# Performance work log

Hardware: AMD Instinct MI355X
Metric: run time of the kernel (lower is better)

Reference implementation:

```python
import jax, jax.numpy as jnp
import numpy as np

W = 32            # window_size
HEADS = 8
DH = 64           # dim_head
DIM = 512
NREL = 2 * W - 1  # 63
N = W * W + 1     # 1025 (cls token)
B = 32
EPS = 1e-6
SCALE = DH ** -0.5


def _bias_indices():
    r = np.arange(W)
    gx, gy = np.meshgrid(r, r, indexing='ij')
    grid = np.stack((gx.reshape(-1), gy.reshape(-1)))        # (2, w*w)
    rel = grid[:, :, None] - grid[:, None, :] + (W - 1)       # (2, n, n)
    return (rel[0] * 1 + rel[1] * NREL).astype(np.int32)      # (w*w, w*w)


def setup_inputs() -> dict:
    key = jax.random.key(0)
    ks = jax.random.split(key, 5)
    return {
        'x': jax.random.normal(ks[0], (B, N, DIM), dtype=jnp.float32),
        'w_qkv': jax.random.normal(ks[1], (DIM, 3 * HEADS * DH), dtype=jnp.float32) * 0.02,
        'g': jnp.ones((DH,), dtype=jnp.float32),                      # RMSNorm scale
        'pe_table': jax.random.normal(ks[2], (NREL * NREL, HEADS), dtype=jnp.float32) * 0.02,
        'w_out': jax.random.normal(ks[3], (HEADS * DH, DIM), dtype=jnp.float32) * 0.02,
        'b_out': jnp.zeros((DIM,), dtype=jnp.float32),
        'bias_idx': jnp.asarray(_bias_indices()),
    }


def _rmsnorm(t, g):
    return t * jax.lax.rsqrt(jnp.mean(t * t, axis=-1, keepdims=True) + EPS) * g


def reference(x, w_qkv, g, pe_table, w_out, b_out, bias_idx):
    b, n, _ = x.shape
    # qkv projection; chunk(3) on last dim == leading axis of (3, H, DH)
    qkv = (x @ w_qkv).reshape(b, n, 3, HEADS, DH)
    qkv = jnp.transpose(qkv, (2, 0, 3, 1, 4))                 # (3, b, h, n, d)
    q, k, v = qkv[0], qkv[1], qkv[2]
    dots = jnp.einsum('bhid,bhjd->bhij', _rmsnorm(q, g), _rmsnorm(k, g)) * SCALE
    bias = jnp.transpose(pe_table[bias_idx], (2, 0, 1))       # (h, w*w, w*w)
    dots = dots.at[:, :, 1:, 1:].add(bias)                    # skip cls row/col
    attn = jax.nn.softmax(dots, axis=-1)
    out = jnp.einsum('bhij,bhjd->bhid', attn, v)
    out = jnp.transpose(out, (0, 2, 1, 3)).reshape(b, n, HEADS * DH)
    return out @ w_out + b_out
```

## Files before the change

kernel.cpp:

```cpp
#include <hip/hip_runtime.h>

typedef short bf16x8 __attribute__((ext_vector_type(8)));
typedef float f32x4 __attribute__((ext_vector_type(4)));
typedef float f32x16 __attribute__((ext_vector_type(16)));
typedef unsigned int u32;
typedef u32 u32x4 __attribute__((ext_vector_type(4)));
typedef unsigned short u16;

#define B_    32
#define N_    1025
#define H_    8
#define DIM_  512
#define M_    (B_*N_)
#define QP_   1152
#define BIP_  1152
#define NT_   34
#define KVSZ_ (NT_*2048)
#define BT_   (BIP_*32)
#define SCALE_ 0.125f
#define LOG2E_ 1.4426950408889634f

__device__ __forceinline__ u16 f2bf(float f){
  unsigned u = __builtin_bit_cast(unsigned, f);
  u += 0x7FFFu + ((u >> 16) & 1u);
  return (u16)(u >> 16);
}
__device__ __forceinline__ u32 cvtpk(float a, float b){
  u32 r;
  asm("v_cvt_pk_bf16_f32 %0, %1, %2" : "=v"(r) : "v"(a), "v"(b));
  return r;
}
__device__ __forceinline__ void pswap(u32 &a, u32 &b){
  asm("v_permlane32_swap_b32 %0, %1" : "+v"(a), "+v"(b));
}
__device__ __forceinline__ void gll16(const u16* g, u16* l){
  __builtin_amdgcn_global_load_lds((const __attribute__((address_space(1))) u16*)(g),
                                   (__attribute__((address_space(3))) u16*)(l), 16, 0, 0);
}

__global__ __launch_bounds__(256)
void k_conv_x(const float* __restrict__ x, u16* __restrict__ o, int n4){
  int i = blockIdx.x*256 + threadIdx.x;
  if (i >= n4) return;
  float4 v = ((const float4*)x)[i];
  ushort4 r;
  r.x = f2bf(v.x); r.y = f2bf(v.y); r.z = f2bf(v.z); r.w = f2bf(v.w);
  ((ushort4*)o)[i] = r;
}

__global__ __launch_bounds__(256)
void k_transpose(const float* __restrict__ w, u16* __restrict__ wt, int R, int C){
  int i = blockIdx.x*256 + threadIdx.x;
  if (i >= R*C) return;
  int n = i / R, k = i - n*R;
  wt[i] = f2bf(w[k*C + n]);
}

__global__ __launch_bounds__(256)
void k_biasr(const int* __restrict__ idx, const float* __restrict__ pe, u16* __restrict__ br){
  int i_lin = blockIdx.x*256 + threadIdx.x;
  int v = i_lin & 15, hi = (i_lin>>4)&1;
  int t1 = i_lin >> 5;
  int i = t1 % 1152;
  int t2 = t1 / 1152;
  int tj = t2 % NT_;
  int h = t2 / NT_;
  int j = tj*32 + (v&3) + 8*(v>>2) + 4*hi;
  float val;
  if (j >= 1 && j <= 1024 && i >= 1 && i <= 1024)
    val = pe[idx[(i-1)*1024 + (j-1)]*8 + h] * LOG2E_;
  else
    val = (j <= 1024) ? 0.f : -1e9f;
  br[i_lin] = f2bf(val);
}

__global__ __launch_bounds__(256)
void k_ztail(u16* __restrict__ qn, u16* __restrict__ kn2, u16* __restrict__ v2){
  int i = blockIdx.x*256 + threadIdx.x;
  if (i < 2080768){
    int bh = i / (127*64); int r = i - bh*(127*64);
    qn[((size_t)bh*QP_ + 1025 + (r>>6))*64 + (r&63)] = 0;
  } else if (i < 2588672){
    int k = i - 2080768; int bh = k/1984; int r = k - bh*1984;
    int n = 1025 + (r>>6), d = r & 63;
    kn2[(size_t)bh*KVSZ_ + 65536 + ((d>>3)<<8) + ((n&31)<<3) + (d&7)] = 0;
  } else if (i < 3096576){
    int k = i - 2588672; int bh = k/1984; int r = k - bh*1984;
    int n = 1025 + (r>>6), d = r & 63;
    v2[(size_t)bh*KVSZ_ + 65536 + (((n>>3)&3)<<9) + (d<<3) + (n&7)] = 0;
  }
}

__global__ __launch_bounds__(256)
void k_qkv(const u16* __restrict__ xb, const u16* __restrict__ wT, const float* __restrict__ g,
           u16* __restrict__ qn, u16* __restrict__ kn2, u16* __restrict__ v2){
  __shared__ u16 sh[16384];
  const int tid = threadIdx.x;
  const int lane = tid & 63, wid = tid >> 6;
  const int lg = lane >> 4, lr = lane & 15;
  const int wm = wid >> 1, wn = wid & 1;

  int orig = blockIdx.x;
  int xcd = orig & 7, idx = orig >> 3;
  int wgid = (xcd < 4 ? xcd*386 : 1544 + (xcd-4)*385) + idx;
  int mt = wgid / 12, nt = wgid - mt*12;
  const int m0 = mt*128, n0 = nt*128;
  const int qkv_t = nt >> 2;
  const int h = ((nt & 3) << 1) + wn;

  const int srow = tid >> 2;
  const int schunk = (tid & 3) ^ ((tid >> 3) & 3);
  const u16* asrc = xb + (size_t)(m0 + srow)*DIM_ + schunk*8;
  const u16* bsrc = wT + (size_t)(n0 + srow)*DIM_ + schunk*8;
  const int rsw = (lg ^ ((lr>>1)&3)) << 3;

  u16* As = sh;
  u16* Bs = sh + 8192;

  f32x4 acc[4][4];
#pragma unroll
  for (int m=0;m<4;++m)
#pragma unroll
    for (int n=0;n<4;++n) acc[m][n] = {0.f,0.f,0.f,0.f};

  gll16(asrc,            As + wid*512);
  gll16(asrc + 64*DIM_,  As + 2048 + wid*512);
  gll16(bsrc,            Bs + wid*512);
  gll16(bsrc + 64*DIM_,  Bs + 2048 + wid*512);

  for (int s=0; s<16; ++s){
    const int cur = s & 1;
    __syncthreads();
    if (s < 15){
      const int ko = (s+1)*32;
      gll16(asrc + ko,           As + (cur^1)*4096 + wid*512);
      gll16(asrc + ko + 64*DIM_, As + (cur^1)*4096 + 2048 + wid*512);
      gll16(bsrc + ko,           Bs + (cur^1)*4096 + wid*512);
      gll16(bsrc + ko + 64*DIM_, Bs + (cur^1)*4096 + 2048 + wid*512);
    }
    bf16x8 af[4], bf[4];
#pragma unroll
    for (int m=0;m<4;++m) af[m] = *(const bf16x8*)(As + cur*4096 + (64*wm+16*m+lr)*32 + rsw);
#pragma unroll
    for (int n=0;n<4;++n) bf[n] = *(const bf16x8*)(Bs + cur*4096 + (64*wn+16*n+lr)*32 + rsw);
    __builtin_amdgcn_s_setprio(1);
#pragma unroll
    for (int m=0;m<4;++m)
#pragma unroll
      for (int n=0;n<4;++n)
        acc[m][n] = __builtin_amdgcn_mfma_f32_16x16x32_bf16(af[m], bf[n], acc[m][n], 0, 0, 0);
    __builtin_amdgcn_s_setprio(0);
  }

  float gv[4];
#pragma unroll
  for (int n=0;n<4;++n)
    gv[n] = (qkv_t==0) ? g[16*n+lr]*(SCALE_*LOG2E_) : (qkv_t==1 ? g[16*n+lr] : 1.f);

#pragma unroll
  for (int m=0;m<4;++m){
    float rstd[4];
    if (qkv_t < 2){
#pragma unroll
      for (int r=0;r<4;++r){
        float s = 0.f;
#pragma unroll
        for (int n=0;n<4;++n) s += acc[m][n][r]*acc[m][n][r];
        s += __shfl_xor(s, 1); s += __shfl_xor(s, 2);
        s += __shfl_xor(s, 4); s += __shfl_xor(s, 8);
        rstd[r] = rsqrtf(s*(1.f/64.f) + 1e-6f);
      }
    } else {
#pragma unroll
      for (int r=0;r<4;++r) rstd[r] = 1.f;
    }
#pragma unroll
    for (int r=0;r<4;++r){
      int mg = m0 + 64*wm + 16*m + 4*lg + r;
      if (mg < M_){
        int b = mg / N_, pos = mg - b*N_;
        int bh = b*H_ + h;
#pragma unroll
        for (int n=0;n<4;++n){
          int d = 16*n + lr;
          u16 val = f2bf(acc[m][n][r]*rstd[r]*gv[n]);
          if (qkv_t == 0)
            qn[((size_t)bh*QP_ + pos)*64 + d] = val;
          else if (qkv_t == 1)
            kn2[(size_t)bh*KVSZ_ + (pos>>5)*2048 + ((d>>3)<<8) + ((pos&31)<<3) + (d&7)] = val;
          else
            v2[(size_t)bh*KVSZ_ + (pos>>5)*2048 + (((pos>>3)&3)<<9) + (d<<3) + (pos&7)] = val;
        }
      }
    }
  }
}

#define TILE(buf, off, B0, B1) do { \
  f32x16 s; \
  _Pragma("unroll") \
  for (int r=0;r<16;++r){ \
    u16 bv = (r < 8) ? ((u16)(B0)[r]) : ((u16)(B1)[r-8]); \
    s[r] = __builtin_bit_cast(float, ((u32)bv) << 16); \
  } \
  __builtin_amdgcn_s_setprio(1); \
  _Pragma("unroll") \
  for (int c=0;c<4;++c){ \
    bf16x8 kf = *(const bf16x8*)(&Ks[buf][0] + (off) + (2*c + hi)*256 + il*8); \
    s = __builtin_amdgcn_mfma_f32_32x32x16_bf16(kf, qf[c], s, 0, 0, 0); \
  } \
  __builtin_amdgcn_s_setprio(0); \
  _Pragma("unroll") \
  for (int r=0;r<16;++r) s[r] = __builtin_amdgcn_exp2f(s[r]); \
  u32 X0 = cvtpk(s[0],s[1]),   X1 = cvtpk(s[2],s[3]); \
  u32 Y0 = cvtpk(s[4],s[5]),   Y1 = cvtpk(s[6],s[7]); \
  u32 X2 = cvtpk(s[8],s[9]),   X3 = cvtpk(s[10],s[11]); \
  u32 Y2 = cvtpk(s[12],s[13]), Y3 = cvtpk(s[14],s[15]); \
  pswap(X0, Y0); pswap(X1, Y1); pswap(X2, Y2); pswap(X3, Y3); \
  u32x4 w0 = {X0, X1, Y0, Y1}; \
  u32x4 w1 = {X2, X3, Y2, Y3}; \
  bf16x8 pv0 = __builtin_bit_cast(bf16x8, w0); \
  bf16x8 pv1 = __builtin_bit_cast(bf16x8, w1); \
  __builtin_amdgcn_s_setprio(1); \
  _Pragma("unroll") \
  for (int c2=0;c2<2;++c2){ \
    bf16x8 pv = c2 ? pv1 : pv0; \
    const u16* vb = &Vs[buf][0] + (off) + (2*c2 + hi)*512; \
    bf16x8 vfA = *(const bf16x8*)(vb + il*8); \
    bf16x8 vfB = *(const bf16x8*)(vb + 256 + il*8); \
    oA = __builtin_amdgcn_mfma_f32_32x32x16_bf16(vfA, pv, oA, 0, 0, 0); \
    oB = __builtin_amdgcn_mfma_f32_32x32x16_bf16(vfB, pv, oB, 0, 0, 0); \
    oS = __builtin_amdgcn_mfma_f32_32x32x16_bf16(onesf, pv, oS, 0, 0, 0); \
  } \
  __builtin_amdgcn_s_setprio(0); \
} while(0)

__global__ __launch_bounds__(256, 3)
void k_attn2(const u16* __restrict__ qn, const u16* __restrict__ kn2, const u16* __restrict__ v2,
             const u16* __restrict__ br, u16* __restrict__ ao){
  __shared__ u16 Ks[2][4096];
  __shared__ u16 Vs[2][4096];
  const int tid = threadIdx.x;
  const int lane = tid & 63, wave = tid >> 6;
  const int il = lane & 31, hi = lane >> 5;
  int wg = ((blockIdx.x & 7) * 288) + (blockIdx.x >> 3);
  int h = wg / 288;
  int rem = wg - h*288;
  int b = rem / 9, qt = rem - (rem/9)*9;
  int bh = b*8 + h;
  int i0 = qt*128 + wave*32;

  const u16* qp = qn + ((size_t)bh*QP_ + (i0 + il))*64 + hi*8;
  bf16x8 qf[4];
#pragma unroll
  for (int c=0;c<4;++c) qf[c] = *(const bf16x8*)(qp + 16*c);

  const u16* ksrc = kn2 + (size_t)bh*KVSZ_ + tid*8;
  const u16* vsrc = v2  + (size_t)bh*KVSZ_ + tid*8;

  gll16(ksrc,        &Ks[0][wave*512]);
  gll16(ksrc + 2048, &Ks[0][2048 + wave*512]);
  gll16(vsrc,        &Vs[0][wave*512]);
  gll16(vsrc + 2048, &Vs[0][2048 + wave*512]);

  f32x16 oA, oB, oS;
#pragma unroll
  for (int r=0;r<16;++r){ oA[r]=0.f; oB[r]=0.f; oS[r]=0.f; }

  const bf16x8 onesf = {0x3F80,0x3F80,0x3F80,0x3F80,0x3F80,0x3F80,0x3F80,0x3F80};

  const u16* bptr = br + ((size_t)(h*NT_)*BIP_ + (i0 + il))*32 + hi*16;
  bf16x8 cb0 = *(const bf16x8*)(bptr);
  bf16x8 cb1 = *(const bf16x8*)(bptr + 8);
  bf16x8 cb2 = *(const bf16x8*)(bptr + BT_);
  bf16x8 cb3 = *(const bf16x8*)(bptr + BT_ + 8);

  for (int t=0; t<16; ++t){
    const int cur = t & 1;
    __syncthreads();
    {
      const int base = (2*t+2)*2048;
      gll16(ksrc + base,        &Ks[cur^1][wave*512]);
      gll16(ksrc + base + 2048, &Ks[cur^1][2048 + wave*512]);
      gll16(vsrc + base,        &Vs[cur^1][wave*512]);
      gll16(vsrc + base + 2048, &Vs[cur^1][2048 + wave*512]);
    }
    TILE(cur, 0, cb0, cb1);
    cb0 = *(const bf16x8*)(bptr + 2*BT_);
    cb1 = *(const bf16x8*)(bptr + 2*BT_ + 8);
    TILE(cur, 2048, cb2, cb3);
    cb2 = *(const bf16x8*)(bptr + 3*BT_);
    cb3 = *(const bf16x8*)(bptr + 3*BT_ + 8);
    bptr += 2*BT_;
  }
  __syncthreads();
  TILE(0, 0, cb0, cb1);

  int i = i0 + il;
  if (i < N_){
    float inv = 1.f / oS[0];
    u16* op = ao + ((size_t)(b*N_ + i))*DIM_ + h*64;
#pragma unroll
    for (int q=0;q<4;++q)
#pragma unroll
      for (int pr=0;pr<2;++pr){
        int d0 = 8*q + 4*hi + 2*pr;
        u32 wA = cvtpk(oA[4*q+2*pr]*inv, oA[4*q+2*pr+1]*inv);
        u32 wB = cvtpk(oB[4*q+2*pr]*inv, oB[4*q+2*pr+1]*inv);
        *(u32*)(op + d0) = wA;
        *(u32*)(op + 32 + d0) = wB;
      }
  }
}

__global__ __launch_bounds__(256)
void k_oproj(const u16* __restrict__ ab, const u16* __restrict__ wT, const float* __restrict__ bo,
             float* __restrict__ out){
  __shared__ u16 sh[16384];
  const int tid = threadIdx.x;
  const int lane = tid & 63, wid = tid >> 6;
  const int lg = lane >> 4, lr = lane & 15;
  const int wm = wid >> 1, wn = wid & 1;

  int orig = blockIdx.x;
  int xcd = orig & 7, idx = orig >> 3;
  int wgid = (xcd < 4 ? xcd*129 : 516 + (xcd-4)*128) + idx;
  int mt = wgid >> 2, nt = wgid & 3;
  const int m0 = mt*128, n0 = nt*128;

  const int srow = tid >> 2;
  const int schunk = (tid & 3) ^ ((tid >> 3) & 3);
  const u16* asrc = ab + (size_t)(m0 + srow)*DIM_ + schunk*8;
  const u16* bsrc = wT + (size_t)(n0 + srow)*DIM_ + schunk*8;
  const int rsw = (lg ^ ((lr>>1)&3)) << 3;

  u16* As = sh;
  u16* Bs = sh + 8192;

  f32x4 acc[4][4];
#pragma unroll
  for (int m=0;m<4;++m)
#pragma unroll
    for (int n=0;n<4;++n) acc[m][n] = {0.f,0.f,0.f,0.f};

  gll16(asrc,            As + wid*512);
  gll16(asrc + 64*DIM_,  As + 2048 + wid*512);
  gll16(bsrc,            Bs + wid*512);
  gll16(bsrc + 64*DIM_,  Bs + 2048 + wid*512);

  for (int s=0; s<16; ++s){
    const int cur = s & 1;
    __syncthreads();
    if (s < 15){
      const int ko = (s+1)*32;
      gll16(asrc + ko,           As + (cur^1)*4096 + wid*512);
      gll16(asrc + ko + 64*DIM_, As + (cur^1)*4096 + 2048 + wid*512);
      gll16(bsrc + ko,           Bs + (cur^1)*4096 + wid*512);
      gll16(bsrc + ko + 64*DIM_, Bs + (cur^1)*4096 + 2048 + wid*512);
    }
    bf16x8 af[4], bf[4];
#pragma unroll
    for (int m=0;m<4;++m) af[m] = *(const bf16x8*)(As + cur*4096 + (64*wm+16*m+lr)*32 + rsw);
#pragma unroll
    for (int n=0;n<4;++n) bf[n] = *(const bf16x8*)(Bs + cur*4096 + (64*wn+16*n+lr)*32 + rsw);
    __builtin_amdgcn_s_setprio(1);
#pragma unroll
    for (int m=0;m<4;++m)
#pragma unroll
      for (int n=0;n<4;++n)
        acc[m][n] = __builtin_amdgcn_mfma_f32_16x16x32_bf16(af[m], bf[n], acc[m][n], 0, 0, 0);
    __builtin_amdgcn_s_setprio(0);
  }

  float bb[4];
#pragma unroll
  for (int n=0;n<4;++n) bb[n] = bo[n0 + 64*wn + 16*n + lr];
#pragma unroll
  for (int m=0;m<4;++m)
#pragma unroll
    for (int r=0;r<4;++r){
      int mg = m0 + 64*wm + 16*m + 4*lg + r;
      if (mg < M_){
#pragma unroll
        for (int n=0;n<4;++n)
          out[(size_t)mg*DIM_ + n0 + 64*wn + 16*n + lr] = acc[m][n][r] + bb[n];
      }
    }
}

extern "C" void kernel_launch(void* const* d_in, const int* in_sizes, int n_in,
                              void* d_out, int out_size, void* d_ws, size_t ws_size,
                              hipStream_t stream) {
  const float* x     = (const float*)d_in[0];
  const float* w_qkv = (const float*)d_in[1];
  const float* g     = (const float*)d_in[2];
  const float* pe    = (const float*)d_in[3];
  const float* w_out = (const float*)d_in[4];
  const float* b_out = (const float*)d_in[5];
  const int*   bidx  = (const int*)d_in[6];
  float* out = (float*)d_out;

  char* ws = (char*)d_ws;
  u16* xb    = (u16*)(ws);
  u16* wT    = (u16*)(ws + 33587200);
  u16* woT   = (u16*)(ws + 35160064);
  u16* qnb   = (u16*)(ws + 35684352);
  u16* kn2   = (u16*)(ws + 73433088);
  u16* v2    = (u16*)(ws + 109084672);
  u16* biasr = (u16*)(ws + 144736256);
  u16* aob   = xb;

  int n4 = (B_*N_*DIM_)/4;
  k_conv_x<<<(n4+255)/256, 256, 0, stream>>>(x, xb, n4);
  k_transpose<<<(1536*512+255)/256, 256, 0, stream>>>(w_qkv, wT, 512, 1536);
  k_transpose<<<(512*512+255)/256, 256, 0, stream>>>(w_out, woT, 512, 512);
  k_biasr<<<39168, 256, 0, stream>>>(bidx, pe, biasr);
  k_ztail<<<12096, 256, 0, stream>>>(qnb, kn2, v2);

  k_qkv<<<3084, 256, 0, stream>>>(xb, wT, g, qnb, kn2, v2);
  k_attn2<<<2304, 256, 0, stream>>>(qnb, kn2, v2, biasr, aob);
  k_oproj<<<1028, 256, 0, stream>>>(aob, woT, b_out, out);
}
```

Before: 295.7 us.

## Fuse preprocessing kernels into one launch, skip padded query waves, raise qkv occupancy

Merges the five preprocessing kernels (x conversion, two weight transposes, bias table build, tail zeroing) into a single k_prep launch to cut launch overhead and inter-kernel gaps. In the attention kernel, waves whose query rows are entirely padding skip the tile compute while still taking part in the barriers and loads. It also adds a min-blocks-per-CU hint of 4 to k_qkv, which may force register spilling.

```diff
diff --git a/kernel.cpp b/kernel.cpp
--- a/kernel.cpp
+++ b/kernel.cpp
@@ -20,6 +20,13 @@
 #define SCALE_ 0.125f
 #define LOG2E_ 1.4426950408889634f
 
+#define CONVN_ (M_*DIM_/4)
+#define TQKV_  (512*1536)
+#define TOUT_  (512*512)
+#define NBIAS_ (8*NT_*1152*32)
+#define NZT_   3096576
+#define PREP_TOTAL_ (CONVN_+TQKV_+TOUT_+NBIAS_+NZT_)
+
 __device__ __forceinline__ u16 f2bf(float f){
   unsigned u = __builtin_bit_cast(unsigned, f);
   u += 0x7FFFu + ((u >> 16) & 1u);
@@ -39,59 +46,59 @@
 }
 
 __global__ __launch_bounds__(256)
-void k_conv_x(const float* __restrict__ x, u16* __restrict__ o, int n4){
+void k_prep(const float* __restrict__ x, const float* __restrict__ wqkv,
+            const float* __restrict__ wout, const int* __restrict__ idx,
+            const float* __restrict__ pe,
+            u16* __restrict__ xb, u16* __restrict__ wT, u16* __restrict__ woT,
+            u16* __restrict__ br,
+            u16* __restrict__ qn, u16* __restrict__ kn2, u16* __restrict__ v2){
   int i = blockIdx.x*256 + threadIdx.x;
-  if (i >= n4) return;
-  float4 v = ((const float4*)x)[i];
-  ushort4 r;
-  r.x = f2bf(v.x); r.y = f2bf(v.y); r.z = f2bf(v.z); r.w = f2bf(v.w);
-  ((ushort4*)o)[i] = r;
-}
-
-__global__ __launch_bounds__(256)
-void k_transpose(const float* __restrict__ w, u16* __restrict__ wt, int R, int C){
-  int i = blockIdx.x*256 + threadIdx.x;
-  if (i >= R*C) return;
-  int n = i / R, k = i - n*R;
-  wt[i] = f2bf(w[k*C + n]);
-}
-
-__global__ __launch_bounds__(256)
-void k_biasr(const int* __restrict__ idx, const float* __restrict__ pe, u16* __restrict__ br){
-  int i_lin = blockIdx.x*256 + threadIdx.x;
-  int v = i_lin & 15, hi = (i_lin>>4)&1;
-  int t1 = i_lin >> 5;
-  int i = t1 % 1152;
-  int t2 = t1 / 1152;
-  int tj = t2 % NT_;
-  int h = t2 / NT_;
-  int j = tj*32 + (v&3) + 8*(v>>2) + 4*hi;
-  float val;
-  if (j >= 1 && j <= 1024 && i >= 1 && i <= 1024)
-    val = pe[idx[(i-1)*1024 + (j-1)]*8 + h] * LOG2E_;
-  else
-    val = (j <= 1024) ? 0.f : -1e9f;
-  br[i_lin] = f2bf(val);
-}
-
-__global__ __launch_bounds__(256)
-void k_ztail(u16* __restrict__ qn, u16* __restrict__ kn2, u16* __restrict__ v2){
-  int i = blockIdx.x*256 + threadIdx.x;
-  if (i < 2080768){
-    int bh = i / (127*64); int r = i - bh*(127*64);
-    qn[((size_t)bh*QP_ + 1025 + (r>>6))*64 + (r&63)] = 0;
-  } else if (i < 2588672){
-    int k = i - 2080768; int bh = k/1984; int r = k - bh*1984;
-    int n = 1025 + (r>>6), d = r & 63;
-    kn2[(size_t)bh*KVSZ_ + 65536 + ((d>>3)<<8) + ((n&31)<<3) + (d&7)] = 0;
-  } else if (i < 3096576){
-    int k = i - 2588672; int bh = k/1984; int r = k - bh*1984;
-    int n = 1025 + (r>>6), d = r & 63;
-    v2[(size_t)bh*KVSZ_ + 65536 + (((n>>3)&3)<<9) + (d<<3) + (n&7)] = 0;
-  }
-}
-
-__global__ __launch_bounds__(256)
+  if (i < CONVN_){
+    float4 v = ((const float4*)x)[i];
+    ushort4 r;
+    r.x = f2bf(v.x); r.y = f2bf(v.y); r.z = f2bf(v.z); r.w = f2bf(v.w);
+    ((ushort4*)xb)[i] = r;
+  } else if (i < CONVN_+TQKV_){
+    int j = i - CONVN_;
+    int n = j / 512, k = j - n*512;
+    wT[j] = f2bf(wqkv[k*1536 + n]);
+  } else if (i < CONVN_+TQKV_+TOUT_){
+    int j = i - (CONVN_+TQKV_);
+    int n = j / 512, k = j - n*512;
+    woT[j] = f2bf(wout[k*512 + n]);
+  } else if (i < CONVN_+TQKV_+TOUT_+NBIAS_){
+    int j = i - (CONVN_+TQKV_+TOUT_);
+    int v = j & 15, hi = (j>>4)&1;
+    int t1 = j >> 5;
+    int ii = t1 % 1152;
+    int t2 = t1 / 1152;
+    int tj = t2 % NT_;
+    int h = t2 / NT_;
+    int jj = tj*32 + (v&3) + 8*(v>>2) + 4*hi;
+    float val;
+    if (jj >= 1 && jj <= 1024 && ii >= 1 && ii <= 1024)
+      val = pe[idx[(ii-1)*1024 + (jj-1)]*8 + h] * LOG2E_;
+    else
+      val = (jj <= 1024) ? 0.f : -1e9f;
+    br[j] = f2bf(val);
+  } else {
+    int j = i - (CONVN_+TQKV_+TOUT_+NBIAS_);
+    if (j < 2080768){
+      int bh = j / (127*64); int r = j - bh*(127*64);
+      qn[((size_t)bh*QP_ + 1025 + (r>>6))*64 + (r&63)] = 0;
+    } else if (j < 2588672){
+      int k = j - 2080768; int bh = k/1984; int r = k - bh*1984;
+      int n = 1025 + (r>>6), d = r & 63;
+      kn2[(size_t)bh*KVSZ_ + 65536 + ((d>>3)<<8) + ((n&31)<<3) + (d&7)] = 0;
+    } else if (j < 3096576){
+      int k = j - 2588672; int bh = k/1984; int r = k - bh*1984;
+      int n = 1025 + (r>>6), d = r & 63;
+      v2[(size_t)bh*KVSZ_ + 65536 + (((n>>3)&3)<<9) + (d<<3) + (n&7)] = 0;
+    }
+  }
+}
+
+__global__ __launch_bounds__(256, 4)
 void k_qkv(const u16* __restrict__ xb, const u16* __restrict__ wT, const float* __restrict__ g,
            u16* __restrict__ qn, u16* __restrict__ kn2, u16* __restrict__ v2){
   __shared__ u16 sh[16384];
@@ -249,6 +256,7 @@
   int b = rem / 9, qt = rem - (rem/9)*9;
   int bh = b*8 + h;
   int i0 = qt*128 + wave*32;
+  const bool active = (i0 <= 1024);
 
   const u16* qp = qn + ((size_t)bh*QP_ + (i0 + il))*64 + hi*8;
   bf16x8 qf[4];
@@ -285,16 +293,20 @@
       gll16(vsrc + base,        &Vs[cur^1][wave*512]);
       gll16(vsrc + base + 2048, &Vs[cur^1][2048 + wave*512]);
     }
-    TILE(cur, 0, cb0, cb1);
-    cb0 = *(const bf16x8*)(bptr + 2*BT_);
-    cb1 = *(const bf16x8*)(bptr + 2*BT_ + 8);
-    TILE(cur, 2048, cb2, cb3);
-    cb2 = *(const bf16x8*)(bptr + 3*BT_);
-    cb3 = *(const bf16x8*)(bptr + 3*BT_ + 8);
-    bptr += 2*BT_;
+    if (active){
+      TILE(cur, 0, cb0, cb1);
+      cb0 = *(const bf16x8*)(bptr + 2*BT_);
+      cb1 = *(const bf16x8*)(bptr + 2*BT_ + 8);
+      TILE(cur, 2048, cb2, cb3);
+      cb2 = *(const bf16x8*)(bptr + 3*BT_);
+      cb3 = *(const bf16x8*)(bptr + 3*BT_ + 8);
+      bptr += 2*BT_;
+    }
   }
   __syncthreads();
-  TILE(0, 0, cb0, cb1);
+  if (active){
+    TILE(0, 0, cb0, cb1);
+  }
 
   int i = i0 + il;
   if (i < N_){
@@ -401,22 +413,17 @@
   float* out = (float*)d_out;
 
   char* ws = (char*)d_ws;
-  u16* xb    = (u16*)(ws);
-  u16* wT    = (u16*)(ws + 33587200);
-  u16* woT   = (u16*)(ws + 35160064);
-  u16* qnb   = (u16*)(ws + 35684352);
-  u16* kn2   = (u16*)(ws + 73433088);
-  u16* v2    = (u16*)(ws + 109084672);
-  u16* biasr = (u16*)(ws + 144736256);
-  u16* aob   = xb;
-
-  int n4 = (B_*N_*DIM_)/4;
-  k_conv_x<<<(n4+255)/256, 256, 0, stream>>>(x, xb, n4);
-  k_transpose<<<(1536*512+255)/256, 256, 0, stream>>>(w_qkv, wT, 512, 1536);
-  k_transpose<<<(512*512+255)/256, 256, 0, stream>>>(w_out, woT, 512, 512);
-  k_biasr<<<39168, 256, 0, stream>>>(bidx, pe, biasr);
-  k_ztail<<<12096, 256, 0, stream>>>(qnb, kn2, v2);
-
+  u16*   xb    = (u16*)(ws);
+  u16*   wT    = (u16*)(ws + 33587200);
+  u16*   woT   = (u16*)(ws + 35160064);
+  u16*   qnb   = (u16*)(ws + 35684352);
+  u16*   kn2   = (u16*)(ws + 73433088);
+  u16*   v2    = (u16*)(ws + 109084672);
+  u16*   biasr = (u16*)(ws + 144736256);
+  u16*   aob   = xb;
+
+  k_prep<<<PREP_TOTAL_/256, 256, 0, stream>>>(x, w_qkv, w_out, bidx, pe,
+                                              xb, wT, woT, biasr, qnb, kn2, v2);
   k_qkv<<<3084, 256, 0, stream>>>(xb, wT, g, qnb, kn2, v2);
   k_attn2<<<2304, 256, 0, stream>>>(qnb, kn2, v2, biasr, aob);
   k_oproj<<<1028, 256, 0, stream>>>(aob, woT, b_out, out);
```

Result: faster. 275.6 us (-6.8%).
